# Kernel tuning notes

Measured on AMD Instinct MI355X. Metric: run time of the kernel, lower is better.

Reference implementation:

```python
import jax, jax.numpy as jnp
import numpy as np

B, S, D, H, FF, P = 16, 200, 512, 8, 2048, 10
HD = D // H
EPS = 1e-5


def _pe2d(h, w, ch):
    # Faithful numpy port of PositionalEncoding2D (positional_encodings lib)
    channels = int(np.ceil(ch / 4) * 2)
    inv_freq = 1.0 / (10000.0 ** (np.arange(0, channels, 2, dtype=np.float32) / channels))
    sin_x = np.einsum('i,j->ij', np.arange(h, dtype=np.float32), inv_freq)
    sin_y = np.einsum('i,j->ij', np.arange(w, dtype=np.float32), inv_freq)
    emb_x = np.stack([np.sin(sin_x), np.cos(sin_x)], -1).reshape(h, channels)
    emb_y = np.stack([np.sin(sin_y), np.cos(sin_y)], -1).reshape(w, channels)
    emb = np.zeros((h, w, 2 * channels), dtype=np.float32)
    emb[:, :, :channels] = emb_x[:, None, :]
    emb[:, :, channels:2 * channels] = emb_y[None, :, :]
    return emb[:, :, :ch]


def _xavier(key, shape):
    fan_out, fan_in = shape
    lim = float(np.sqrt(6.0 / (fan_in + fan_out)))
    return jax.random.uniform(key, shape, minval=-lim, maxval=lim, dtype=jnp.float32)


def setup_inputs():
    key = jax.random.key(0)
    ks = jax.random.split(key, 8)
    x = jax.random.normal(ks[0], (B, S, D), dtype=jnp.float32)
    pos = jnp.asarray(_pe2d(S, S, P))  # (S, S, P) positional bias features
    Wkv = _xavier(ks[1], (2 * D, D)); bkv = jnp.zeros((2 * D,))
    Wo = _xavier(ks[2], (D, D)); bo = jnp.zeros((D,))
    Wpos = _xavier(ks[3], (1, P)); bpos = jnp.zeros((1,))
    W1 = _xavier(ks[4], (FF, D)); b1 = jnp.zeros((FF,))
    W2 = _xavier(ks[5], (D, FF)); b2 = jnp.zeros((D,))
    g1 = jnp.ones((D,)); beta1 = jnp.zeros((D,))
    g2 = jnp.ones((D,)); beta2 = jnp.zeros((D,))
    return {"x": x, "pos": pos, "Wkv": Wkv, "bkv": bkv, "Wo": Wo, "bo": bo,
            "Wpos": Wpos, "bpos": bpos, "W1": W1, "b1": b1, "W2": W2, "b2": b2,
            "g1": g1, "beta1": beta1, "g2": g2, "beta2": beta2}


def _layernorm(x, g, b):
    mu = jnp.mean(x, axis=-1, keepdims=True)
    var = jnp.mean(jnp.square(x - mu), axis=-1, keepdims=True)
    return (x - mu) * jax.lax.rsqrt(var + EPS) * g + b


def reference(x, pos, Wkv, bkv, Wo, bo, Wpos, bpos, W1, b1, W2, b2, g1, beta1, g2, beta2):
    # --- MultiheadAttention_KV (attn_type='kv') ---
    kv = x @ Wkv.T + bkv                                   # (B,S,2D)
    kv = kv.reshape(B, S, H, 2 * HD).transpose(0, 2, 1, 3)  # (B,H,S,2hd)
    k, v = kv[..., :HD], kv[..., HD:]
    attn = jnp.einsum('bhid,bhjd->bhij', k, k) / jnp.sqrt(jnp.float32(HD))
    # map_pos is linear: map_pos(attn[...,None] + pos) == attn*sum(w) + (pos@w + b)
    # -> same math as materializing the (B,H,S,S,P) tensor, but fused.
    pos_bias = pos @ Wpos[0] + bpos[0]                     # (S,S)
    scores = attn * jnp.sum(Wpos) + pos_bias[None, None]
    a = jax.nn.softmax(scores, axis=-1)
    vals = jnp.einsum('bhij,bhjd->bhid', a, v)             # (B,H,S,hd)
    vals = vals.transpose(0, 2, 1, 3).reshape(B, S, D)
    o = vals @ Wo.T + bo
    # --- residual + post-norm ---
    h = _layernorm(x + o, g1, beta1)
    # --- FFN ---
    ff = jax.nn.relu(h @ W1.T + b1) @ W2.T + b2
    return _layernorm(h + ff, g2, beta2)
```

## Files before the change

### kernel.cpp

```cpp
#include <hip/hip_runtime.h>
#include <hip/hip_bf16.h>

#define EPSV 1e-5f
static const int B_ = 16, S_ = 200, D_ = 512, H_ = 8, FF_ = 2048, P_ = 10, HD_ = 64;
static const int SP = 224;

typedef __bf16 bf16_t;
typedef __attribute__((ext_vector_type(8))) __bf16 bf16x8;
typedef __attribute__((ext_vector_type(4))) __bf16 bf16x4;
typedef __attribute__((ext_vector_type(4))) float f32x4;

__device__ __forceinline__ void gload16(const void* g, void* l) {
    __builtin_amdgcn_global_load_lds(
        (const __attribute__((address_space(1))) void*)g,
        (__attribute__((address_space(3))) void*)l, 16, 0, 0);
}

template <int BM, int BN, int WROWS, int WCOLS, int EPI, int NSPLIT>
__global__ __launch_bounds__(256) void mfma_gemm(
    const bf16_t* __restrict__ A,
    const bf16_t* __restrict__ Bw,
    float* __restrict__ Cf, bf16_t* __restrict__ Cb, long cBat, int ldc,
    const float* __restrict__ bias,
    bf16_t* __restrict__ kOut, bf16_t* __restrict__ vtOut,
    int M, int N, int K)
{
    constexpr int MR = WROWS / 16, NR = WCOLS / 16;
    constexpr int NWC = BN / WCOLS;
    static_assert((4 / NWC) * WROWS == BM, "wave tiling must cover BM");
    static_assert(NWC * WCOLS == BN, "wave tiling must cover BN");

    __shared__ bf16_t Asm[BM * 64];
    __shared__ bf16_t Bsm[BN * 64];

    const int wv = threadIdx.x >> 6;
    const int ln = threadIdx.x & 63;
    const int split = blockIdx.z % NSPLIT;
    const int rowBase = blockIdx.y * BM;
    const int colBase = blockIdx.x * BN;
    const int wr = (wv / NWC) * WROWS;
    const int wc = (wv % NWC) * WCOLS;

    const int lr8 = ln >> 3;
    const int lc = (ln & 7) * 8;

    f32x4 acc[MR][NR] = {};

    const int kBeg = split * (K / NSPLIT);
    const int kEnd = kBeg + K / NSPLIT;

    for (int k0 = kBeg; k0 < kEnd; k0 += 64) {
        #pragma unroll
        for (int i = 0; i < BM / 32; i++) {
            int row = i * 32 + wv * 8 + lr8;
            int gr = rowBase + row; gr = (gr < M) ? gr : (M - 1);
            gload16(A + (long)gr * K + k0 + lc, &Asm[(i * 32 + wv * 8) * 64]);
        }
        #pragma unroll
        for (int i = 0; i < BN / 32; i++) {
            int col = i * 32 + wv * 8 + lr8;
            int gc = colBase + col; gc = (gc < N) ? gc : (N - 1);
            gload16(Bw + (long)gc * K + k0 + lc, &Bsm[(i * 32 + wv * 8) * 64]);
        }
        __syncthreads();

        #pragma unroll
        for (int kk = 0; kk < 2; kk++) {
            bf16x8 af[MR], bfr[NR];
            #pragma unroll
            for (int m = 0; m < MR; m++)
                af[m] = *reinterpret_cast<const bf16x8*>(
                    &Asm[(wr + m * 16 + (ln & 15)) * 64 + kk * 32 + (ln >> 4) * 8]);
            #pragma unroll
            for (int n = 0; n < NR; n++)
                bfr[n] = *reinterpret_cast<const bf16x8*>(
                    &Bsm[(wc + n * 16 + (ln & 15)) * 64 + kk * 32 + (ln >> 4) * 8]);
            #pragma unroll
            for (int m = 0; m < MR; m++)
                #pragma unroll
                for (int n = 0; n < NR; n++)
                    acc[m][n] = __builtin_amdgcn_mfma_f32_16x16x32_bf16(
                        af[m], bfr[n], acc[m][n], 0, 0, 0);
        }
        __syncthreads();
    }

    #pragma unroll
    for (int m = 0; m < MR; m++) {
        #pragma unroll
        for (int n = 0; n < NR; n++) {
            #pragma unroll
            for (int r = 0; r < 4; r++) {
                int row = rowBase + wr + m * 16 + (ln >> 4) * 4 + r;
                int col = colBase + wc + n * 16 + (ln & 15);
                if (row >= M || col >= N) continue;
                float v = acc[m][n][r];
                if constexpr (EPI == 3) {
                    v += bias[col];
                    int b = row / S_, s = row - b * S_;
                    int h = col >> 7, w = col & 127;
                    if (w < HD_)
                        kOut[((long)(b * H_ + h) * SP + s) * HD_ + w] = (bf16_t)v;
                    else
                        vtOut[((long)(b * H_ + h) * HD_ + (w - HD_)) * SP + s] = (bf16_t)v;
                } else if constexpr (EPI == 1) {
                    v += bias[col];
                    v = fmaxf(v, 0.f);
                    Cb[(long)row * ldc + col] = (bf16_t)v;
                } else {
                    Cf[(long)split * cBat + (long)row * ldc + col] = v;
                }
            }
        }
    }
}

__global__ __launch_bounds__(256) void attn_fused(
    const bf16_t* __restrict__ Kb, const bf16_t* __restrict__ Vt,
    const float* __restrict__ G, const float* __restrict__ scalePtr,
    bf16_t* __restrict__ vals)
{
    __shared__ __align__(16) bf16_t Pl[4][16][232];

    const int bh = blockIdx.x;
    const int tile = blockIdx.y;
    const int wv = threadIdx.x >> 6;
    const int ln = threadIdx.x & 63;
    const int b = bh >> 3, h = bh & 7;
    const int rowBase = tile * 64 + wv * 16;

    const bf16_t* Kbh = Kb + (long)bh * SP * HD_;
    const bf16_t* Vbh = Vt + (long)bh * HD_ * SP;
    const float scale = scalePtr[0];

    const int lr = ln & 15;
    const int lk = (ln >> 4) * 8;

    f32x4 acc[14];
    #pragma unroll
    for (int n = 0; n < 14; n++) acc[n] = (f32x4){0.f, 0.f, 0.f, 0.f};

    int arow = rowBase + lr; arow = (arow < S_) ? arow : (S_ - 1);
    const bf16x8 a0 = *reinterpret_cast<const bf16x8*>(Kbh + (long)arow * HD_ + lk);
    const bf16x8 a1 = *reinterpret_cast<const bf16x8*>(Kbh + (long)arow * HD_ + 32 + lk);

    #pragma unroll
    for (int n = 0; n < 14; n++) {
        const bf16_t* bp = Kbh + (long)(n * 16 + lr) * HD_;
        bf16x8 b0 = *reinterpret_cast<const bf16x8*>(bp + lk);
        bf16x8 b1 = *reinterpret_cast<const bf16x8*>(bp + 32 + lk);
        acc[n] = __builtin_amdgcn_mfma_f32_16x16x32_bf16(a0, b0, acc[n], 0, 0, 0);
        acc[n] = __builtin_amdgcn_mfma_f32_16x16x32_bf16(a1, b1, acc[n], 0, 0, 0);
    }

    float Gc[14];
    #pragma unroll
    for (int n = 0; n < 14; n++) Gc[n] = G[n * 16 + lr];

    #pragma unroll
    for (int r = 0; r < 4; r++) {
        float m = -1e30f;
        #pragma unroll
        for (int n = 0; n < 14; n++) {
            float v = acc[n][r] * scale + Gc[n];
            acc[n][r] = v;
            m = fmaxf(m, v);
        }
        #pragma unroll
        for (int off = 1; off < 16; off <<= 1) m = fmaxf(m, __shfl_xor(m, off));
        float s = 0.f;
        #pragma unroll
        for (int n = 0; n < 14; n++) {
            float e = __expf(acc[n][r] - m);
            acc[n][r] = e;
            s += e;
        }
        #pragma unroll
        for (int off = 1; off < 16; off <<= 1) s += __shfl_xor(s, off);
        float inv = 1.f / s;
        #pragma unroll
        for (int n = 0; n < 14; n++) acc[n][r] *= inv;
    }

    #pragma unroll
    for (int n = 0; n < 14; n++)
        #pragma unroll
        for (int r = 0; r < 4; r++)
            Pl[wv][(ln >> 4) * 4 + r][n * 16 + lr] = (bf16_t)acc[n][r];

    f32x4 vacc[4] = {};
    #pragma unroll
    for (int kk = 0; kk < 7; kk++) {
        bf16x8 pa = *reinterpret_cast<const bf16x8*>(&Pl[wv][lr][kk * 32 + lk]);
        #pragma unroll
        for (int n = 0; n < 4; n++) {
            bf16x8 vb = *reinterpret_cast<const bf16x8*>(
                Vbh + (long)(n * 16 + lr) * SP + kk * 32 + lk);
            vacc[n] = __builtin_amdgcn_mfma_f32_16x16x32_bf16(pa, vb, vacc[n], 0, 0, 0);
        }
    }

    #pragma unroll
    for (int n = 0; n < 4; n++) {
        #pragma unroll
        for (int r = 0; r < 4; r++) {
            int row = rowBase + (ln >> 4) * 4 + r;
            if (row < S_)
                vals[((long)b * S_ + row) * D_ + h * HD_ + n * 16 + lr] =
                    (bf16_t)vacc[n][r];
        }
    }
}

__global__ __launch_bounds__(256) void convert_all(
    const float* __restrict__ x, const float* __restrict__ Wkv,
    const float* __restrict__ Wo, const float* __restrict__ W1,
    const float* __restrict__ W2, bf16_t* __restrict__ dst)
{
    const int tot = 1130496;
    for (int i = blockIdx.x * blockDim.x + threadIdx.x; i < tot;
         i += gridDim.x * blockDim.x) {
        long e = (long)i * 4;
        const float* s; long off;
        if (e < 1638400)      { s = x;   off = e; }
        else if (e < 2162688) { s = Wkv; off = e - 1638400; }
        else if (e < 2424832) { s = Wo;  off = e - 2162688; }
        else if (e < 3473408) { s = W1;  off = e - 2424832; }
        else                  { s = W2;  off = e - 3473408; }
        float4 v = *reinterpret_cast<const float4*>(s + off);
        bf16x4 o = {(bf16_t)v.x, (bf16_t)v.y, (bf16_t)v.z, (bf16_t)v.w};
        *reinterpret_cast<bf16x4*>(dst + e) = o;
    }
}

__global__ __launch_bounds__(256) void zero_f4(float4* __restrict__ p, int n4)
{
    int i = blockIdx.x * blockDim.x + threadIdx.x;
    if (i < n4) p[i] = make_float4(0.f, 0.f, 0.f, 0.f);
}

__global__ void prep_g(const float* __restrict__ pos, const float* __restrict__ Wpos,
                       float* __restrict__ G, float* __restrict__ scal)
{
    int t = threadIdx.x;
    if (t < SP) {
        float g = -1e30f;
        if (t < S_) {
            g = 0.f;
            #pragma unroll
            for (int p = 6; p < 10; p++) g += pos[(long)t * P_ + p] * Wpos[p];
        }
        G[t] = g;
    }
    if (t == 0) {
        float sw = 0.f;
        for (int p = 0; p < P_; p++) sw += Wpos[p];
        scal[0] = sw * 0.125f;
    }
}

template <int NPART>
__global__ __launch_bounds__(256) void add_ln_p(
    const float* __restrict__ a, const float* __restrict__ parts, long partStride,
    const float* __restrict__ bias,
    const float* __restrict__ g, const float* __restrict__ beta,
    float* __restrict__ outf, bf16_t* __restrict__ outb, int rows)
{
    int row = blockIdx.x * 4 + (threadIdx.x >> 6);
    int lane = threadIdx.x & 63;
    if (row >= rows) return;
    long base = (long)row * D_;
    float v[8];
    float sum = 0.f;
    #pragma unroll
    for (int i = 0; i < 8; i++) {
        int c = lane + i * 64;
        float t = a[base + c] + bias[c];
        #pragma unroll
        for (int p = 0; p < NPART; p++) t += parts[p * partStride + base + c];
        v[i] = t;
        sum += t;
    }
    #pragma unroll
    for (int off = 32; off; off >>= 1) sum += __shfl_xor(sum, off);
    float mean = sum * (1.f / 512.f);
    float var = 0.f;
    #pragma unroll
    for (int i = 0; i < 8; i++) { float d = v[i] - mean; var += d * d; }
    #pragma unroll
    for (int off = 32; off; off >>= 1) var += __shfl_xor(var, off);
    float rstd = rsqrtf(var * (1.f / 512.f) + EPSV);
    #pragma unroll
    for (int i = 0; i < 8; i++) {
        int c = lane + i * 64;
        float o = (v[i] - mean) * rstd * g[c] + beta[c];
        outf[base + c] = o;
        if (outb) outb[base + c] = (bf16_t)o;
    }
}

extern "C" void kernel_launch(void* const* d_in, const int* in_sizes, int n_in,
                              void* d_out, int out_size, void* d_ws, size_t ws_size,
                              hipStream_t stream)
{
    const float* x    = (const float*)d_in[0];
    const float* pos  = (const float*)d_in[1];
    const float* Wkv  = (const float*)d_in[2];
    const float* bkv  = (const float*)d_in[3];
    const float* Wo   = (const float*)d_in[4];
    const float* bo   = (const float*)d_in[5];
    const float* Wpos = (const float*)d_in[6];
    const float* bpos = (const float*)d_in[7];
    const float* W1   = (const float*)d_in[8];
    const float* b1   = (const float*)d_in[9];
    const float* W2   = (const float*)d_in[10];
    const float* b2   = (const float*)d_in[11];
    const float* g1   = (const float*)d_in[12];
    const float* be1  = (const float*)d_in[13];
    const float* g2   = (const float*)d_in[14];
    const float* be2  = (const float*)d_in[15];
    (void)bpos;
    float* out = (float*)d_out;

    char* w = (char*)d_ws;
    bf16_t* xb   = (bf16_t*)(w + 0);
    bf16_t* Wkvb = (bf16_t*)(w + 3276800);
    bf16_t* Wob  = (bf16_t*)(w + 4325376);
    bf16_t* W1b  = (bf16_t*)(w + 4849664);
    bf16_t* W2b  = (bf16_t*)(w + 6946816);
    bf16_t* Kb   = (bf16_t*)(w + 9043968);
    bf16_t* Vt   = (bf16_t*)(w + 12713984);
    float*  G    = (float*)(w + 16384000);
    float*  scal = (float*)(w + 16384896);
    bf16_t* vals = (bf16_t*)(w + 16385024);
    float*  hf   = (float*)(w + 19661824);
    bf16_t* hb   = (bf16_t*)(w + 26215424);
    float*  obuf = (float*)(w + 29492224);
    bf16_t* tb   = (bf16_t*)(w + 42599424);
    float*  fbuf = (float*)(w + 55706624);

    const int M = B_ * S_;
    const long PS = (long)M * D_;

    convert_all<<<2048, 256, 0, stream>>>(x, Wkv, Wo, W1, W2, xb);
    zero_f4<<<1792, 256, 0, stream>>>((float4*)Kb, 458752);
    prep_g<<<1, 256, 0, stream>>>(pos, Wpos, G, scal);

    mfma_gemm<64, 128, 32, 64, 3, 1><<<dim3(8, 50, 1), 256, 0, stream>>>(
        xb, Wkvb, nullptr, nullptr, 0, 0, bkv, Kb, Vt, M, 2 * D_, D_);

    attn_fused<<<dim3(128, 4, 1), 256, 0, stream>>>(Kb, Vt, G, scal, vals);

    mfma_gemm<64, 64, 32, 32, 5, 2><<<dim3(8, 50, 2), 256, 0, stream>>>(
        vals, Wob, obuf, nullptr, PS, D_, nullptr, nullptr, nullptr, M, D_, D_);

    add_ln_p<2><<<(M + 3) / 4, 256, 0, stream>>>(x, obuf, PS, bo, g1, be1, hf, hb, M);

    mfma_gemm<64, 128, 32, 64, 1, 1><<<dim3(16, 50, 1), 256, 0, stream>>>(
        hb, W1b, nullptr, tb, 0, FF_, b1, nullptr, nullptr, M, FF_, D_);

    mfma_gemm<64, 64, 32, 32, 5, 4><<<dim3(8, 50, 4), 256, 0, stream>>>(
        tb, W2b, fbuf, nullptr, PS, D_, nullptr, nullptr, nullptr, M, D_, FF_);

    add_ln_p<4><<<(M + 3) / 4, 256, 0, stream>>>(hf, fbuf, PS, b2, g2, be2, out, nullptr, M);
}
```

Measured before the change: 117.4 us.

## Double-buffer GEMM LDS tiles, merge prep kernels, shrink GEMM tiles

The GEMM now keeps two LDS buffers and issues the global-to-LDS load for the next K chunk before computing the current one. This drops one barrier per iteration and overlaps load latency with MFMA work. The three setup kernels (convert, zero, prep_g) are merged into one launch to save launch overhead. The KV and FFN1 GEMMs move to 64x64 tiles with twice as many blocks, which raises parallelism but lowers per-block data reuse.

```diff
diff --git a/kernel.cpp b/kernel.cpp
--- a/kernel.cpp
+++ b/kernel.cpp
@@ -16,7 +16,7 @@
         (__attribute__((address_space(3))) void*)l, 16, 0, 0);
 }
 
-template <int BM, int BN, int WROWS, int WCOLS, int EPI, int NSPLIT>
+template <int BM, int BN, int WROWS, int WCOLS, int EPI, int NSPLIT, int KC>
 __global__ __launch_bounds__(256) void mfma_gemm(
     const bf16_t* __restrict__ A,
     const bf16_t* __restrict__ Bw,
@@ -27,15 +27,16 @@
 {
     constexpr int MR = WROWS / 16, NR = WCOLS / 16;
     constexpr int NWC = BN / WCOLS;
+    constexpr int NIT = KC / 64;
     static_assert((4 / NWC) * WROWS == BM, "wave tiling must cover BM");
     static_assert(NWC * WCOLS == BN, "wave tiling must cover BN");
 
-    __shared__ bf16_t Asm[BM * 64];
-    __shared__ bf16_t Bsm[BN * 64];
+    __shared__ bf16_t Asm[2][BM * 64];
+    __shared__ bf16_t Bsm[2][BN * 64];
 
     const int wv = threadIdx.x >> 6;
     const int ln = threadIdx.x & 63;
-    const int split = blockIdx.z % NSPLIT;
+    const int split = blockIdx.z;
     const int rowBase = blockIdx.y * BM;
     const int colBase = blockIdx.x * BN;
     const int wr = (wv / NWC) * WROWS;
@@ -43,38 +44,37 @@
 
     const int lr8 = ln >> 3;
     const int lc = (ln & 7) * 8;
+    const int kBeg = split * KC;
 
     f32x4 acc[MR][NR] = {};
 
-    const int kBeg = split * (K / NSPLIT);
-    const int kEnd = kBeg + K / NSPLIT;
-
-    for (int k0 = kBeg; k0 < kEnd; k0 += 64) {
+    auto STAGE = [&](int k0, int buf) {
         #pragma unroll
         for (int i = 0; i < BM / 32; i++) {
             int row = i * 32 + wv * 8 + lr8;
             int gr = rowBase + row; gr = (gr < M) ? gr : (M - 1);
-            gload16(A + (long)gr * K + k0 + lc, &Asm[(i * 32 + wv * 8) * 64]);
+            gload16(A + (long)gr * K + k0 + lc, &Asm[buf][(i * 32 + wv * 8) * 64]);
         }
         #pragma unroll
         for (int i = 0; i < BN / 32; i++) {
             int col = i * 32 + wv * 8 + lr8;
             int gc = colBase + col; gc = (gc < N) ? gc : (N - 1);
-            gload16(Bw + (long)gc * K + k0 + lc, &Bsm[(i * 32 + wv * 8) * 64]);
-        }
-        __syncthreads();
-
+            gload16(Bw + (long)gc * K + k0 + lc, &Bsm[buf][(i * 32 + wv * 8) * 64]);
+        }
+    };
+
+    auto COMPUTE = [&](int buf) {
         #pragma unroll
         for (int kk = 0; kk < 2; kk++) {
             bf16x8 af[MR], bfr[NR];
             #pragma unroll
             for (int m = 0; m < MR; m++)
                 af[m] = *reinterpret_cast<const bf16x8*>(
-                    &Asm[(wr + m * 16 + (ln & 15)) * 64 + kk * 32 + (ln >> 4) * 8]);
+                    &Asm[buf][(wr + m * 16 + (ln & 15)) * 64 + kk * 32 + (ln >> 4) * 8]);
             #pragma unroll
             for (int n = 0; n < NR; n++)
                 bfr[n] = *reinterpret_cast<const bf16x8*>(
-                    &Bsm[(wc + n * 16 + (ln & 15)) * 64 + kk * 32 + (ln >> 4) * 8]);
+                    &Bsm[buf][(wc + n * 16 + (ln & 15)) * 64 + kk * 32 + (ln >> 4) * 8]);
             #pragma unroll
             for (int m = 0; m < MR; m++)
                 #pragma unroll
@@ -82,7 +82,16 @@
                     acc[m][n] = __builtin_amdgcn_mfma_f32_16x16x32_bf16(
                         af[m], bfr[n], acc[m][n], 0, 0, 0);
         }
-        __syncthreads();
+    };
+
+    STAGE(kBeg, 0);
+    __syncthreads();
+
+    #pragma unroll
+    for (int t = 0; t < NIT; t++) {
+        if (t + 1 < NIT) STAGE(kBeg + (t + 1) * 64, (t + 1) & 1);
+        COMPUTE(t & 1);
+        if (t + 1 < NIT) __syncthreads();
     }
 
     #pragma unroll
@@ -212,14 +221,18 @@
     }
 }
 
-__global__ __launch_bounds__(256) void convert_all(
+__global__ __launch_bounds__(256) void prep_all(
     const float* __restrict__ x, const float* __restrict__ Wkv,
     const float* __restrict__ Wo, const float* __restrict__ W1,
-    const float* __restrict__ W2, bf16_t* __restrict__ dst)
-{
-    const int tot = 1130496;
-    for (int i = blockIdx.x * blockDim.x + threadIdx.x; i < tot;
-         i += gridDim.x * blockDim.x) {
+    const float* __restrict__ W2, bf16_t* __restrict__ dst,
+    float4* __restrict__ zeroP,
+    const float* __restrict__ pos, const float* __restrict__ Wpos,
+    float* __restrict__ G, float* __restrict__ scal)
+{
+    const int gid = blockIdx.x * blockDim.x + threadIdx.x;
+    const int nthr = gridDim.x * blockDim.x;
+
+    for (int i = gid; i < 1130496; i += nthr) {
         long e = (long)i * 4;
         const float* s; long off;
         if (e < 1638400)      { s = x;   off = e; }
@@ -231,28 +244,18 @@
         bf16x4 o = {(bf16_t)v.x, (bf16_t)v.y, (bf16_t)v.z, (bf16_t)v.w};
         *reinterpret_cast<bf16x4*>(dst + e) = o;
     }
-}
-
-__global__ __launch_bounds__(256) void zero_f4(float4* __restrict__ p, int n4)
-{
-    int i = blockIdx.x * blockDim.x + threadIdx.x;
-    if (i < n4) p[i] = make_float4(0.f, 0.f, 0.f, 0.f);
-}
-
-__global__ void prep_g(const float* __restrict__ pos, const float* __restrict__ Wpos,
-                       float* __restrict__ G, float* __restrict__ scal)
-{
-    int t = threadIdx.x;
-    if (t < SP) {
+    for (int i = gid; i < 458752; i += nthr)
+        zeroP[i] = make_float4(0.f, 0.f, 0.f, 0.f);
+    if (gid < SP) {
         float g = -1e30f;
-        if (t < S_) {
+        if (gid < S_) {
             g = 0.f;
             #pragma unroll
-            for (int p = 6; p < 10; p++) g += pos[(long)t * P_ + p] * Wpos[p];
-        }
-        G[t] = g;
-    }
-    if (t == 0) {
+            for (int p = 6; p < 10; p++) g += pos[(long)gid * P_ + p] * Wpos[p];
+        }
+        G[gid] = g;
+    }
+    if (gid == 0) {
         float sw = 0.f;
         for (int p = 0; p < P_; p++) sw += Wpos[p];
         scal[0] = sw * 0.125f;
@@ -310,7 +313,6 @@
     const float* Wo   = (const float*)d_in[4];
     const float* bo   = (const float*)d_in[5];
     const float* Wpos = (const float*)d_in[6];
-    const float* bpos = (const float*)d_in[7];
     const float* W1   = (const float*)d_in[8];
     const float* b1   = (const float*)d_in[9];
     const float* W2   = (const float*)d_in[10];
@@ -319,7 +321,6 @@
     const float* be1  = (const float*)d_in[13];
     const float* g2   = (const float*)d_in[14];
     const float* be2  = (const float*)d_in[15];
-    (void)bpos;
     float* out = (float*)d_out;
 
     char* w = (char*)d_ws;
@@ -342,24 +343,23 @@
     const int M = B_ * S_;
     const long PS = (long)M * D_;
 
-    convert_all<<<2048, 256, 0, stream>>>(x, Wkv, Wo, W1, W2, xb);
-    zero_f4<<<1792, 256, 0, stream>>>((float4*)Kb, 458752);
-    prep_g<<<1, 256, 0, stream>>>(pos, Wpos, G, scal);
-
-    mfma_gemm<64, 128, 32, 64, 3, 1><<<dim3(8, 50, 1), 256, 0, stream>>>(
+    prep_all<<<2048, 256, 0, stream>>>(x, Wkv, Wo, W1, W2, xb, (float4*)Kb,
+                                       pos, Wpos, G, scal);
+
+    mfma_gemm<64, 64, 32, 32, 3, 1, 512><<<dim3(16, 50, 1), 256, 0, stream>>>(
         xb, Wkvb, nullptr, nullptr, 0, 0, bkv, Kb, Vt, M, 2 * D_, D_);
 
     attn_fused<<<dim3(128, 4, 1), 256, 0, stream>>>(Kb, Vt, G, scal, vals);
 
-    mfma_gemm<64, 64, 32, 32, 5, 2><<<dim3(8, 50, 2), 256, 0, stream>>>(
+    mfma_gemm<64, 64, 32, 32, 5, 2, 256><<<dim3(8, 50, 2), 256, 0, stream>>>(
         vals, Wob, obuf, nullptr, PS, D_, nullptr, nullptr, nullptr, M, D_, D_);
 
     add_ln_p<2><<<(M + 3) / 4, 256, 0, stream>>>(x, obuf, PS, bo, g1, be1, hf, hb, M);
 
-    mfma_gemm<64, 128, 32, 64, 1, 1><<<dim3(16, 50, 1), 256, 0, stream>>>(
+    mfma_gemm<64, 64, 32, 32, 1, 1, 512><<<dim3(32, 50, 1), 256, 0, stream>>>(
         hb, W1b, nullptr, tb, 0, FF_, b1, nullptr, nullptr, M, FF_, D_);
 
-    mfma_gemm<64, 64, 32, 32, 5, 4><<<dim3(8, 50, 4), 256, 0, stream>>>(
+    mfma_gemm<64, 64, 32, 32, 5, 4, 512><<<dim3(8, 50, 4), 256, 0, stream>>>(
         tb, W2b, fbuf, nullptr, PS, D_, nullptr, nullptr, nullptr, M, D_, FF_);
 
     add_ln_p<4><<<(M + 3) / 4, 256, 0, stream>>>(hf, fbuf, PS, b2, g2, be2, out, nullptr, M);
```

Result: no change. 118.8 us (+1.1%).
